# Optimization experiments

Measured on AMD Instinct MI355X. Metric: run time of the kernel, lower is better.

## Reference

```python
import jax, jax.numpy as jnp
import numpy as np


def _max_agg_conv(x, w, b, src, dst, num_nodes):
    # Linear transform then gather along source nodes and scatter-max to targets.
    h = x @ w.T + b                      # [N, out]
    msgs = h[src]                        # [E, out] edge messages (x_j)
    agg = jax.ops.segment_max(msgs, dst, num_segments=num_nodes)  # [N, out]
    # torch_scatter / PyG fill isolated nodes with 0, jax fills with -inf
    return jnp.where(jnp.isneginf(agg), jnp.zeros((), agg.dtype), agg)


def setup_inputs() -> dict:
    key = jax.random.key(0)
    k_x, k_e, k_w1, k_b1, k_w2, k_b2 = jax.random.split(key, 6)
    N, E = 100000, 1600000
    IN, HID, OUT = 128, 32, 32
    x = jax.random.normal(k_x, (N, IN), dtype=jnp.float32)
    edge_index = jax.random.randint(k_e, (2, E), 0, N, dtype=jnp.int64)
    s1 = 1.0 / np.sqrt(IN)
    s2 = 1.0 / np.sqrt(HID)
    w1 = jax.random.uniform(k_w1, (HID, IN), jnp.float32, -s1, s1)
    b1 = jax.random.uniform(k_b1, (HID,), jnp.float32, -s1, s1)
    w2 = jax.random.uniform(k_w2, (OUT, HID), jnp.float32, -s2, s2)
    b2 = jax.random.uniform(k_b2, (OUT,), jnp.float32, -s2, s2)
    return {"x": x, "edge_index": edge_index, "w1": w1, "b1": b1, "w2": w2, "b2": b2}


def reference(x, edge_index, w1, b1, w2, b2):
    num_nodes = x.shape[0]
    src, dst = edge_index[0], edge_index[1]
    h = _max_agg_conv(x, w1, b1, src, dst, num_nodes)   # conv1
    h = jax.nn.relu(h)
    out = _max_agg_conv(h, w2, b2, src, dst, num_nodes)  # conv2
    return out
```

## Files before the change

kernel.cpp:

```cpp
#include <hip/hip_runtime.h>
#include <math.h>


#define NPB 512
#define BSHIFT 9
#define CAP 32
#define CCH 2048
#define BPAD 16

typedef __attribute__((ext_vector_type(8))) short bf16x8;
typedef __attribute__((ext_vector_type(4))) float f32x4;

__global__ __launch_bounds__(256) void fill_s32_kernel(int* __restrict__ p, int v, int n) {
    int i = blockIdx.x * 256 + threadIdx.x;
    if (i < n) p[i] = v;
}

__global__ __launch_bounds__(256) void hist_buckets_kernel(
    const int* __restrict__ dst, int* __restrict__ bcnt, int B, int E)
{
    __shared__ int lc[256];
    const int tid = threadIdx.x;
    lc[tid] = 0;
    __syncthreads();
    for (int e = blockIdx.x * 256 + tid; e < E; e += gridDim.x * 256)
        atomicAdd(&lc[dst[e] >> BSHIFT], 1);
    __syncthreads();
    if (tid < B && lc[tid]) atomicAdd(&bcnt[tid * BPAD], lc[tid]);
}

__global__ __launch_bounds__(256) void bucket_scan_kernel(
    int* __restrict__ bcur, int* __restrict__ bbase, int* __restrict__ of_cnt,
    int B, int E)
{
    __shared__ int sh[256];
    const int tid = threadIdx.x;
    int v = (tid < B) ? bcur[tid * BPAD] : 0;
    sh[tid] = v;
    __syncthreads();
    #pragma unroll
    for (int d = 1; d < 256; d <<= 1) {
        int t = (tid >= d) ? sh[tid - d] : 0;
        __syncthreads();
        sh[tid] += t;
        __syncthreads();
    }
    if (tid < B) { int b = sh[tid] - v; bbase[tid] = b; bcur[tid * BPAD] = b; }
    if (tid == 0) { bbase[B] = E; *of_cnt = 0; }
}

__global__ __launch_bounds__(256) void partition_kernel(
    const int* __restrict__ src, const int* __restrict__ dst,
    int* __restrict__ bcur, uint2* __restrict__ pairs, int E)
{
    __shared__ uint2 stage[CCH];
    __shared__ int lcnt[256], loffs[256], lcur[256], gb[256], sh[256];
    const int tid = threadIdx.x;
    const int e0 = blockIdx.x * CCH;
    const int ecnt = min(CCH, E - e0);
    lcnt[tid] = 0;
    __syncthreads();
    for (int i = tid; i < ecnt; i += 256)
        atomicAdd(&lcnt[dst[e0 + i] >> BSHIFT], 1);
    __syncthreads();
    int v = lcnt[tid];
    sh[tid] = v;
    __syncthreads();
    #pragma unroll
    for (int d = 1; d < 256; d <<= 1) {
        int t = (tid >= d) ? sh[tid - d] : 0;
        __syncthreads();
        sh[tid] += t;
        __syncthreads();
    }
    loffs[tid] = sh[tid] - v;
    lcur[tid] = sh[tid] - v;
    gb[tid] = v ? atomicAdd(&bcur[tid * BPAD], v) : 0;
    __syncthreads();
    for (int i = tid; i < ecnt; i += 256) {
        int d = dst[e0 + i];
        int s = atomicAdd(&lcur[d >> BSHIFT], 1);
        stage[s] = make_uint2((unsigned)src[e0 + i], (unsigned)d);
    }
    __syncthreads();
    for (int i = tid; i < ecnt; i += 256) {
        uint2 p = stage[i];
        int b = (int)(p.y >> BSHIFT);
        pairs[gb[b] + (i - loffs[b])] = p;
    }
}

__global__ __launch_bounds__(256) void build_ell_kernel(
    const uint2* __restrict__ pairs, const int* __restrict__ bbase,
    int* __restrict__ ell, int* __restrict__ cnt,
    uint2* __restrict__ of_list, int* __restrict__ of_cnt, int N, int of_cap)
{
    __shared__ int lcnt[NPB];
    __shared__ int lell[NPB * CAP];
    const int tid = threadIdx.x, b = blockIdx.x;
    for (int i = tid; i < NPB; i += 256) lcnt[i] = 0;
    __syncthreads();
    const int p0 = bbase[b], p1 = bbase[b + 1];
    for (int i = p0 + tid; i < p1; i += 256) {
        uint2 p = pairs[i];
        int ln = (int)p.y - b * NPB;
        int s = atomicAdd(&lcnt[ln], 1);
        if (s < CAP) lell[ln * CAP + s] = (int)p.x;
        else { int oi = atomicAdd(of_cnt, 1); if (oi < of_cap) of_list[oi] = p; }
    }
    __syncthreads();
    const size_t eb = (size_t)b * NPB * CAP;
    for (int i = tid; i < NPB * CAP; i += 256) ell[eb + i] = lell[i];
    const int n0 = b * NPB;
    for (int i = tid; i < NPB; i += 256)
        if (n0 + i < N) cnt[n0 + i] = lcnt[i];
}

__device__ __forceinline__ void split_bf16(float f, unsigned short& hi, unsigned short& lo) {
    unsigned u = __float_as_uint(f);
    hi = (unsigned short)(u >> 16);
    float fh = __uint_as_float(u & 0xffff0000u);
    float r = f - fh;
    lo = (unsigned short)(__float_as_uint(r) >> 16);
}

#define L1S 136
__global__ __launch_bounds__(256) void linear1_mfma_kernel(
    const float* __restrict__ x, const float* __restrict__ w1,
    const float* __restrict__ b1, float* __restrict__ h1, int N)
{
    __shared__ unsigned short xh[64 * L1S];
    __shared__ unsigned short xl[64 * L1S];
    __shared__ unsigned short wh[32 * L1S];
    __shared__ unsigned short wl[32 * L1S];
    const int tid = threadIdx.x;
    const int node0 = blockIdx.x * 64;
    for (int q = tid; q < 32 * 32; q += 256) {
        int row = q >> 5, qc = (q & 31) * 4;
        float4 v = *reinterpret_cast<const float4*>(w1 + row * 128 + qc);
        unsigned short h0, l0, h1s, l1s, h2, l2, h3, l3;
        split_bf16(v.x, h0, l0); split_bf16(v.y, h1s, l1s);
        split_bf16(v.z, h2, l2); split_bf16(v.w, h3, l3);
        short4 hv = {(short)h0, (short)h1s, (short)h2, (short)h3};
        short4 lv = {(short)l0, (short)l1s, (short)l2, (short)l3};
        *reinterpret_cast<short4*>(&wh[row * L1S + qc]) = hv;
        *reinterpret_cast<short4*>(&wl[row * L1S + qc]) = lv;
    }
    for (int q = tid; q < 64 * 32; q += 256) {
        int row = q >> 5, qc = (q & 31) * 4;
        if (node0 + row < N) {
            float4 v = *reinterpret_cast<const float4*>(x + (size_t)(node0 + row) * 128 + qc);
            unsigned short h0, l0, h1s, l1s, h2, l2, h3, l3;
            split_bf16(v.x, h0, l0); split_bf16(v.y, h1s, l1s);
            split_bf16(v.z, h2, l2); split_bf16(v.w, h3, l3);
            short4 hv = {(short)h0, (short)h1s, (short)h2, (short)h3};
            short4 lv = {(short)l0, (short)l1s, (short)l2, (short)l3};
            *reinterpret_cast<short4*>(&xh[row * L1S + qc]) = hv;
            *reinterpret_cast<short4*>(&xl[row * L1S + qc]) = lv;
        }
    }
    __syncthreads();
    const int wid = tid >> 6, lane = tid & 63;
    const int arow = wid * 16 + (lane & 15);
    const int koff = (lane >> 4) * 8;
    bf16x8 ah[4], al[4], bh[2][4], bl[2][4];
    #pragma unroll
    for (int kt = 0; kt < 4; ++kt) {
        ah[kt] = *reinterpret_cast<const bf16x8*>(&xh[arow * L1S + kt * 32 + koff]);
        al[kt] = *reinterpret_cast<const bf16x8*>(&xl[arow * L1S + kt * 32 + koff]);
    }
    #pragma unroll
    for (int nt = 0; nt < 2; ++nt) {
        int ch = nt * 16 + (lane & 15);
        #pragma unroll
        for (int kt = 0; kt < 4; ++kt) {
            bh[nt][kt] = *reinterpret_cast<const bf16x8*>(&wh[ch * L1S + kt * 32 + koff]);
            bl[nt][kt] = *reinterpret_cast<const bf16x8*>(&wl[ch * L1S + kt * 32 + koff]);
        }
    }
    f32x4 acc[2] = {{0.f, 0.f, 0.f, 0.f}, {0.f, 0.f, 0.f, 0.f}};
    #pragma unroll
    for (int nt = 0; nt < 2; ++nt)
        #pragma unroll
        for (int kt = 0; kt < 4; ++kt) {
            acc[nt] = __builtin_amdgcn_mfma_f32_16x16x32_bf16(ah[kt], bh[nt][kt], acc[nt], 0, 0, 0);
            acc[nt] = __builtin_amdgcn_mfma_f32_16x16x32_bf16(ah[kt], bl[nt][kt], acc[nt], 0, 0, 0);
            acc[nt] = __builtin_amdgcn_mfma_f32_16x16x32_bf16(al[kt], bh[nt][kt], acc[nt], 0, 0, 0);
        }
    const int col = lane & 15, r0 = (lane >> 4) * 4;
    #pragma unroll
    for (int nt = 0; nt < 2; ++nt) {
        int ch = nt * 16 + col;
        float bias = b1[ch];
        #pragma unroll
        for (int r = 0; r < 4; ++r) {
            int n = node0 + wid * 16 + r0 + r;
            if (n < N) h1[(size_t)n * 32 + ch] = acc[nt][r] + bias;
        }
    }
}

__global__ __launch_bounds__(256) void linear2_kernel(
    const float* __restrict__ agg1, const float* __restrict__ w2,
    const float* __restrict__ b2, float* __restrict__ h2, int N)
{
    __shared__ float wsh[32][36];
    __shared__ float rs[64][32];
    const int tid = threadIdx.x;
    for (int i = tid; i < 32 * 32; i += 256) wsh[i >> 5][i & 31] = w2[i];
    const int node0 = blockIdx.x * 64;
    const float4* a4 = reinterpret_cast<const float4*>(agg1 + (size_t)node0 * 32);
    for (int q = tid; q < 64 * 8; q += 256) {
        int row = q >> 3;
        if (node0 + row < N) {
            float4 v = a4[q];
            *reinterpret_cast<float4*>(&rs[row][(q & 7) * 4]) = v;
        }
    }
    __syncthreads();
    const int g = tid >> 5, j = tid & 31;
    const int nb = g * 8;
    const float bj = b2[j];
    float acc[8];
    #pragma unroll
    for (int a = 0; a < 8; ++a) acc[a] = bj;
    const float4* wrow = reinterpret_cast<const float4*>(&wsh[j][0]);
    #pragma unroll
    for (int k4 = 0; k4 < 8; ++k4) {
        float4 w = wrow[k4];
        #pragma unroll
        for (int a = 0; a < 8; ++a) {
            float4 xv = *reinterpret_cast<const float4*>(&rs[nb + a][k4 * 4]);
            acc[a] += xv.x * w.x + xv.y * w.y + xv.z * w.z + xv.w * w.w;
        }
    }
    #pragma unroll
    for (int a = 0; a < 8; ++a) {
        int n = node0 + nb + a;
        if (n < N) h2[(size_t)n * 32 + j] = acc[a];
    }
}

__global__ __launch_bounds__(256) void agg_ell_kernel(
    const float* __restrict__ h, const int* __restrict__ cnt,
    const int* __restrict__ ell, float* __restrict__ out,
    int N, float seed, int fixup)
{
    int t = blockIdx.x * 256 + threadIdx.x;
    int n = t >> 3;
    if (n >= N) return;
    int c = (t & 7) << 2;
    int total = cnt[n];
    int deg = min(total, CAP);
    const int* row = ell + (size_t)n * CAP;
    float4 acc = {seed, seed, seed, seed};
    int k = 0;
    for (; k + 1 < deg; k += 2) {
        int s0 = row[k], s1 = row[k + 1];
        float4 v0 = *reinterpret_cast<const float4*>(h + (size_t)s0 * 32 + c);
        float4 v1 = *reinterpret_cast<const float4*>(h + (size_t)s1 * 32 + c);
        acc.x = fmaxf(acc.x, fmaxf(v0.x, v1.x));
        acc.y = fmaxf(acc.y, fmaxf(v0.y, v1.y));
        acc.z = fmaxf(acc.z, fmaxf(v0.z, v1.z));
        acc.w = fmaxf(acc.w, fmaxf(v0.w, v1.w));
    }
    if (k < deg) {
        int s0 = row[k];
        float4 v0 = *reinterpret_cast<const float4*>(h + (size_t)s0 * 32 + c);
        acc.x = fmaxf(acc.x, v0.x);
        acc.y = fmaxf(acc.y, v0.y);
        acc.z = fmaxf(acc.z, v0.z);
        acc.w = fmaxf(acc.w, v0.w);
    }
    if (fixup && total == 0) acc = make_float4(0.f, 0.f, 0.f, 0.f);
    *reinterpret_cast<float4*>(out + (size_t)n * 32 + c) = acc;
}

__device__ __forceinline__ void atomicMaxF(float* a, float v) {
    int* ai = (int*)a;
    int old = *ai;
    while (v > __int_as_float(old)) {
        int assumed = old;
        old = atomicCAS(ai, assumed, __float_as_int(v));
        if (old == assumed) break;
    }
}

__global__ __launch_bounds__(256) void overflow_fixup_kernel(
    const float* __restrict__ h, const uint2* __restrict__ of_list,
    const int* __restrict__ of_cnt, float* __restrict__ out, int of_cap)
{
    int m = min(*of_cnt, of_cap);
    for (int t = blockIdx.x * 256 + threadIdx.x; t < m * 8; t += gridDim.x * 256) {
        int e = t >> 3, c = (t & 7) << 2;
        uint2 p = of_list[e];
        const float* hv = h + (size_t)p.x * 32 + c;
        float* a = out + (size_t)p.y * 32 + c;
        atomicMaxF(a + 0, hv[0]);
        atomicMaxF(a + 1, hv[1]);
        atomicMaxF(a + 2, hv[2]);
        atomicMaxF(a + 3, hv[3]);
    }
}

extern "C" void kernel_launch(void* const* d_in, const int* in_sizes, int n_in,
                              void* d_out, int out_size, void* d_ws, size_t ws_size,
                              hipStream_t stream)
{
    const float* x  = (const float*)d_in[0];
    const int*   ei = (const int*)d_in[1];
    const float* w1 = (const float*)d_in[2];
    const float* b1 = (const float*)d_in[3];
    const float* w2 = (const float*)d_in[4];
    const float* b2 = (const float*)d_in[5];
    float* out = (float*)d_out;

    const int N = in_sizes[0] / 128;
    const int E = in_sizes[1] / 2;
    const int C = (int)((size_t)N * 32);
    const int B = (N + NPB - 1) / NPB;
    const int* src = ei;
    const int* dst = ei + E;

    auto align256 = [](size_t v) { return (v + 255) & ~(size_t)255; };
    size_t off = 0;
    size_t rsize = (size_t)C * 4 > (size_t)E * 8 ? (size_t)C * 4 : (size_t)E * 8;
    char* base = (char*)d_ws;
    uint2* pairs = (uint2*)(base + off);
    float* bufA  = (float*)(base + off);       off = align256(off + rsize);
    float* bufB  = (float*)(base + off);       off = align256(off + (size_t)C * 4);
    int*   ell   = (int*)(base + off);         off = align256(off + (size_t)B * NPB * CAP * 4);
    int*   cnt   = (int*)(base + off);         off = align256(off + (size_t)N * 4);
    int*   bbase = (int*)(base + off);         off = align256(off + (size_t)(B + 1) * 4);
    int*   bcur  = (int*)(base + off);         off = align256(off + (size_t)B * BPAD * 4);
    int*   of_cnt = (int*)(base + off);        off = align256(off + 256);
    uint2* of_list = (uint2*)(base + off);
    size_t rem = (ws_size > off) ? (ws_size - off) / 8 : 0;
    int of_cap = (int)((rem < (size_t)E) ? rem : (size_t)E);

    fill_s32_kernel<<<(B * BPAD + 255) / 256, 256, 0, stream>>>(bcur, 0, B * BPAD);
    hist_buckets_kernel<<<256, 256, 0, stream>>>(dst, bcur, B, E);
    bucket_scan_kernel<<<1, 256, 0, stream>>>(bcur, bbase, of_cnt, B, E);
    partition_kernel<<<(E + CCH - 1) / CCH, 256, 0, stream>>>(src, dst, bcur, pairs, E);
    build_ell_kernel<<<B, 256, 0, stream>>>(pairs, bbase, ell, cnt, of_list, of_cnt, N, of_cap);

    const int aggGrid = (int)(((size_t)N * 8 + 255) / 256);

    linear1_mfma_kernel<<<(N + 63) / 64, 256, 0, stream>>>(x, w1, b1, bufA, N);
    agg_ell_kernel<<<aggGrid, 256, 0, stream>>>(bufA, cnt, ell, bufB, N, 0.0f, 0);
    overflow_fixup_kernel<<<32, 256, 0, stream>>>(bufA, of_list, of_cnt, bufB, of_cap);

    linear2_kernel<<<(N + 63) / 64, 256, 0, stream>>>(bufB, w2, b2, bufA, N);
    agg_ell_kernel<<<aggGrid, 256, 0, stream>>>(bufA, cnt, ell, out, N, -INFINITY, 1);
    overflow_fixup_kernel<<<32, 256, 0, stream>>>(bufA, of_list, of_cnt, out, of_cap);
}
```

Before: 271.6 us.

## Fuse first aggregation with second linear and fold overflow handling into gather

Merges the conv1 ELL max-aggregation with the second linear transform in one kernel, so the intermediate aggregate is kept in shared memory instead of written to and reread from global memory. The separate atomic-CAS overflow kernels are removed. Every node thread now scans the whole overflow list for edges aimed at it, which adds a linear scan per thread and could be costly if overflow is non-empty. The ELL scratch array is also zero-initialised in shared memory.

```diff
diff --git a/kernel.cpp b/kernel.cpp
--- a/kernel.cpp
+++ b/kernel.cpp
@@ -99,6 +99,7 @@
     __shared__ int lell[NPB * CAP];
     const int tid = threadIdx.x, b = blockIdx.x;
     for (int i = tid; i < NPB; i += 256) lcnt[i] = 0;
+    for (int i = tid; i < NPB * CAP; i += 256) lell[i] = 0;
     __syncthreads();
     const int p0 = bbase[b], p1 = bbase[b + 1];
     for (int i = p0 + tid; i < p1; i += 256) {
@@ -200,58 +201,11 @@
     }
 }
 
-__global__ __launch_bounds__(256) void linear2_kernel(
-    const float* __restrict__ agg1, const float* __restrict__ w2,
-    const float* __restrict__ b2, float* __restrict__ h2, int N)
-{
-    __shared__ float wsh[32][36];
-    __shared__ float rs[64][32];
-    const int tid = threadIdx.x;
-    for (int i = tid; i < 32 * 32; i += 256) wsh[i >> 5][i & 31] = w2[i];
-    const int node0 = blockIdx.x * 64;
-    const float4* a4 = reinterpret_cast<const float4*>(agg1 + (size_t)node0 * 32);
-    for (int q = tid; q < 64 * 8; q += 256) {
-        int row = q >> 3;
-        if (node0 + row < N) {
-            float4 v = a4[q];
-            *reinterpret_cast<float4*>(&rs[row][(q & 7) * 4]) = v;
-        }
-    }
-    __syncthreads();
-    const int g = tid >> 5, j = tid & 31;
-    const int nb = g * 8;
-    const float bj = b2[j];
-    float acc[8];
-    #pragma unroll
-    for (int a = 0; a < 8; ++a) acc[a] = bj;
-    const float4* wrow = reinterpret_cast<const float4*>(&wsh[j][0]);
-    #pragma unroll
-    for (int k4 = 0; k4 < 8; ++k4) {
-        float4 w = wrow[k4];
-        #pragma unroll
-        for (int a = 0; a < 8; ++a) {
-            float4 xv = *reinterpret_cast<const float4*>(&rs[nb + a][k4 * 4]);
-            acc[a] += xv.x * w.x + xv.y * w.y + xv.z * w.z + xv.w * w.w;
-        }
-    }
-    #pragma unroll
-    for (int a = 0; a < 8; ++a) {
-        int n = node0 + nb + a;
-        if (n < N) h2[(size_t)n * 32 + j] = acc[a];
-    }
-}
-
-__global__ __launch_bounds__(256) void agg_ell_kernel(
-    const float* __restrict__ h, const int* __restrict__ cnt,
-    const int* __restrict__ ell, float* __restrict__ out,
-    int N, float seed, int fixup)
-{
-    int t = blockIdx.x * 256 + threadIdx.x;
-    int n = t >> 3;
-    if (n >= N) return;
-    int c = (t & 7) << 2;
-    int total = cnt[n];
-    int deg = min(total, CAP);
+__device__ __forceinline__ float4 agg_node(
+    const float* __restrict__ h, const int* __restrict__ ell,
+    const uint2* __restrict__ of_list, int m,
+    int n, int c, int deg, float seed)
+{
     const int* row = ell + (size_t)n * CAP;
     float4 acc = {seed, seed, seed, seed};
     int k = 0;
@@ -272,35 +226,78 @@
         acc.z = fmaxf(acc.z, v0.z);
         acc.w = fmaxf(acc.w, v0.w);
     }
-    if (fixup && total == 0) acc = make_float4(0.f, 0.f, 0.f, 0.f);
+    for (int e = 0; e < m; ++e) {
+        uint2 p = of_list[e];
+        if ((int)p.y == n) {
+            float4 v0 = *reinterpret_cast<const float4*>(h + (size_t)p.x * 32 + c);
+            acc.x = fmaxf(acc.x, v0.x);
+            acc.y = fmaxf(acc.y, v0.y);
+            acc.z = fmaxf(acc.z, v0.z);
+            acc.w = fmaxf(acc.w, v0.w);
+        }
+    }
+    return acc;
+}
+
+__global__ __launch_bounds__(256) void agg1_lin2_kernel(
+    const float* __restrict__ h1, const int* __restrict__ cnt,
+    const int* __restrict__ ell, const uint2* __restrict__ of_list,
+    const int* __restrict__ of_cnt, int of_cap,
+    const float* __restrict__ w2, const float* __restrict__ b2,
+    float* __restrict__ h2, int N)
+{
+    __shared__ float wsh[32][36];
+    __shared__ float a1s[32][36];
+    const int tid = threadIdx.x;
+    for (int i = tid; i < 32 * 32; i += 256) wsh[i >> 5][i & 31] = w2[i];
+    const int node0 = blockIdx.x * 32;
+    const int ln = tid >> 3, c = (tid & 7) << 2;
+    const int n = node0 + ln;
+    const int m = min(*of_cnt, of_cap);
+    float4 acc = {0.f, 0.f, 0.f, 0.f};
+    if (n < N) {
+        int deg = min(cnt[n], CAP);
+        acc = agg_node(h1, ell, of_list, m, n, c, deg, 0.0f);
+    }
+    *reinterpret_cast<float4*>(&a1s[ln][c]) = acc;
+    __syncthreads();
+    const int g = tid >> 5, j = tid & 31;
+    const int nb = g * 4;
+    const float bj = b2[j];
+    float o[4] = {bj, bj, bj, bj};
+    const float4* wrow = reinterpret_cast<const float4*>(&wsh[j][0]);
+    #pragma unroll
+    for (int k4 = 0; k4 < 8; ++k4) {
+        float4 w = wrow[k4];
+        #pragma unroll
+        for (int a = 0; a < 4; ++a) {
+            float4 xv = *reinterpret_cast<const float4*>(&a1s[nb + a][k4 * 4]);
+            o[a] += xv.x * w.x + xv.y * w.y + xv.z * w.z + xv.w * w.w;
+        }
+    }
+    #pragma unroll
+    for (int a = 0; a < 4; ++a) {
+        int nn = node0 + nb + a;
+        if (nn < N) h2[(size_t)nn * 32 + j] = o[a];
+    }
+}
+
+__global__ __launch_bounds__(256) void agg2_kernel(
+    const float* __restrict__ h2, const int* __restrict__ cnt,
+    const int* __restrict__ ell, const uint2* __restrict__ of_list,
+    const int* __restrict__ of_cnt, int of_cap,
+    float* __restrict__ out, int N)
+{
+    int t = blockIdx.x * 256 + threadIdx.x;
+    int n = t >> 3;
+    if (n >= N) return;
+    int c = (t & 7) << 2;
+    const int m = min(*of_cnt, of_cap);
+    int total = cnt[n];
+    int deg = min(total, CAP);
+    float4 acc = agg_node(h2, ell, of_list, m, n, c, deg, -INFINITY);
+    if (total == 0) acc = make_float4(0.f, 0.f, 0.f, 0.f);
     *reinterpret_cast<float4*>(out + (size_t)n * 32 + c) = acc;
-}
-
-__device__ __forceinline__ void atomicMaxF(float* a, float v) {
-    int* ai = (int*)a;
-    int old = *ai;
-    while (v > __int_as_float(old)) {
-        int assumed = old;
-        old = atomicCAS(ai, assumed, __float_as_int(v));
-        if (old == assumed) break;
-    }
-}
-
-__global__ __launch_bounds__(256) void overflow_fixup_kernel(
-    const float* __restrict__ h, const uint2* __restrict__ of_list,
-    const int* __restrict__ of_cnt, float* __restrict__ out, int of_cap)
-{
-    int m = min(*of_cnt, of_cap);
-    for (int t = blockIdx.x * 256 + threadIdx.x; t < m * 8; t += gridDim.x * 256) {
-        int e = t >> 3, c = (t & 7) << 2;
-        uint2 p = of_list[e];
-        const float* hv = h + (size_t)p.x * 32 + c;
-        float* a = out + (size_t)p.y * 32 + c;
-        atomicMaxF(a + 0, hv[0]);
-        atomicMaxF(a + 1, hv[1]);
-        atomicMaxF(a + 2, hv[2]);
-        atomicMaxF(a + 3, hv[3]);
-    }
 }
 
 extern "C" void kernel_launch(void* const* d_in, const int* in_sizes, int n_in,
@@ -344,13 +341,12 @@
     partition_kernel<<<(E + CCH - 1) / CCH, 256, 0, stream>>>(src, dst, bcur, pairs, E);
     build_ell_kernel<<<B, 256, 0, stream>>>(pairs, bbase, ell, cnt, of_list, of_cnt, N, of_cap);
 
-    const int aggGrid = (int)(((size_t)N * 8 + 255) / 256);
+    const int nodeGrid = (N + 31) / 32;
 
     linear1_mfma_kernel<<<(N + 63) / 64, 256, 0, stream>>>(x, w1, b1, bufA, N);
-    agg_ell_kernel<<<aggGrid, 256, 0, stream>>>(bufA, cnt, ell, bufB, N, 0.0f, 0);
-    overflow_fixup_kernel<<<32, 256, 0, stream>>>(bufA, of_list, of_cnt, bufB, of_cap);
-
-    linear2_kernel<<<(N + 63) / 64, 256, 0, stream>>>(bufB, w2, b2, bufA, N);
-    agg_ell_kernel<<<aggGrid, 256, 0, stream>>>(bufA, cnt, ell, out, N, -INFINITY, 1);
-    overflow_fixup_kernel<<<32, 256, 0, stream>>>(bufA, of_list, of_cnt, out, of_cap);
-}
+    agg1_lin2_kernel<<<nodeGrid, 256, 0, stream>>>(
+        bufA, cnt, ell, of_list, of_cnt, of_cap, w2, b2, bufB, N);
+
+    agg2_kernel<<<nodeGrid, 256, 0, stream>>>(
+        bufB, cnt, ell, of_list, of_cnt, of_cap, out, N);
+}
```

After: 268.9 us. About the same (-1.0%).
